# Kernel optimization log

Hardware: AMD Instinct MI355X
Metric: run time of the kernel (lower is better)

The kernel has to match this reference:

```python
import jax, jax.numpy as jnp
import numpy as np

MAX_SENT_LEN = 28
B, LAT, D, E = 2048, 256, 1024, 256
LN_EPS = 1e-5


def setup_inputs() -> dict:
    key = jax.random.key(0)
    ks = jax.random.split(key, 10)
    s = 0.05
    return {
        "z": jax.random.normal(ks[0], (B, LAT), jnp.float32),
        "true_inp": jax.random.normal(ks[1], (B, MAX_SENT_LEN, E), jnp.float32),
        "tf_mask": jax.random.bernoulli(ks[2], 0.5, (MAX_SENT_LEN,)),
        "fc_w": jax.random.normal(ks[3], (D, LAT), jnp.float32) * s,
        "fc_b": jnp.zeros((D,), jnp.float32),
        "ln_w": jnp.ones((D,), jnp.float32),
        "ln_b": jnp.zeros((D,), jnp.float32),
        "w_ih": jax.random.normal(ks[4], (3 * D, D), jnp.float32) * s,
        "b_ih": jnp.zeros((3 * D,), jnp.float32),
        "w_hh": jax.random.normal(ks[5], (3 * D, D), jnp.float32) * s,
        "b_hh": jnp.zeros((3 * D,), jnp.float32),
    }


def reference(z, true_inp, tf_mask, fc_w, fc_b, ln_w, ln_b, w_ih, b_ih, w_hh, b_hh):
    # fc + layer norm -> initial hidden and (repeated) step input, [B, D]
    x = z @ fc_w.T + fc_b
    mu = jnp.mean(x, axis=-1, keepdims=True)
    var = jnp.mean(jnp.square(x - mu), axis=-1, keepdims=True)
    x = (x - mu) * jax.lax.rsqrt(var + LN_EPS) * ln_w + ln_b

    # encoded input is identical at every step -> precompute input gates once
    gi = x @ w_ih.T + b_ih                      # [B, 3D]
    i_r, i_z, i_n = jnp.split(gi, 3, axis=-1)

    # true_inp.repeat(1,1,repeating).transpose(1,0) -> [T, B, D]
    rep = D // E
    true_rep = jnp.transpose(jnp.tile(true_inp, (1, 1, rep)), (1, 0, 2))

    def step(h, inputs):
        t_inp, m = inputs
        h_in = jnp.where(m, t_inp, h)           # teacher-forcing branch
        gh = h_in @ w_hh.T + b_hh               # [B, 3D]
        h_r, h_z, h_n = jnp.split(gh, 3, axis=-1)
        r = jax.nn.sigmoid(i_r + h_r)
        u = jax.nn.sigmoid(i_z + h_z)
        n = jnp.tanh(i_n + r * h_n)
        h_new = (1.0 - u) * n + u * h_in
        return h_new, h_new

    _, outs = jax.lax.scan(step, x, (true_rep, tf_mask))
    return outs                                  # [T, B, D]
```

## Files before the change

### kernel.cpp

```cpp
#include <hip/hip_runtime.h>
#include <hip/hip_bf16.h>

#define TSTEPS 28

typedef __attribute__((ext_vector_type(8))) short bf16x8;
typedef __attribute__((ext_vector_type(4))) float f32x4;
typedef __attribute__((ext_vector_type(4))) unsigned short u16x4;
typedef __hip_bfloat16 bf16;

__device__ __forceinline__ unsigned short f2b(float f) {
  bf16 h = __float2bfloat16(f);
  return *reinterpret_cast<unsigned short*>(&h);
}
__device__ __forceinline__ float b2f(unsigned short u) {
  bf16 h = *reinterpret_cast<bf16*>(&u);
  return __bfloat162float(h);
}

__device__ __forceinline__ void gload16(const void* g, void* l) {
  __builtin_amdgcn_global_load_lds(
      (const __attribute__((address_space(1))) void*)g,
      (__attribute__((address_space(3))) void*)l, 16, 0, 0);
}

__device__ __forceinline__ float sigm(float x) { return 1.f / (1.f + __expf(-x)); }
__device__ __forceinline__ float tanh_fast(float x) {
  const float e2 = __expf(2.f * x);
  return 1.f - 2.f / (e2 + 1.f);
}

__global__ void conv_kernel(const float* __restrict__ in, unsigned short* __restrict__ out, int n4) {
  int i = blockIdx.x * blockDim.x + threadIdx.x;
  const int stride = gridDim.x * blockDim.x;
  for (; i < n4; i += stride) {
    const float4 v = *(const float4*)&in[(size_t)i * 4];
    u16x4 o;
    o.x = f2b(v.x); o.y = f2b(v.y); o.z = f2b(v.z); o.w = f2b(v.w);
    *(u16x4*)&out[(size_t)i * 4] = o;
  }
}

__global__ __launch_bounds__(256) void fold_kernel(const float* __restrict__ whh,
                                                   unsigned short* __restrict__ whf) {
  const int idx = blockIdx.x * 256 + threadIdx.x;
  const int n = idx >> 6, k4 = (idx & 63) << 2;
  const float* r = &whh[(size_t)n * 1024 + k4];
  const float4 a = *(const float4*)r;
  const float4 b = *(const float4*)(r + 256);
  const float4 c = *(const float4*)(r + 512);
  const float4 d = *(const float4*)(r + 768);
  u16x4 o;
  o.x = f2b(a.x + b.x + c.x + d.x);
  o.y = f2b(a.y + b.y + c.y + d.y);
  o.z = f2b(a.z + b.z + c.z + d.z);
  o.w = f2b(a.w + b.w + c.w + d.w);
  *(u16x4*)&whf[(size_t)n * 256 + k4] = o;
}

__global__ __launch_bounds__(256, 2) void gemm_fc_kernel(
    const bf16* __restrict__ A, const bf16* __restrict__ W,
    const float* __restrict__ bias, float* __restrict__ out) {
  constexpr int K = 256, NT = K / 32;
  __shared__ __align__(16) bf16 lds[2][6144];
  const int tid = threadIdx.x;
  const int lane = tid & 63;
  const int l15 = lane & 15, l4 = lane >> 4;
  const int wid = tid >> 6, wm = wid >> 1, wn = wid & 1;
  const int m0 = blockIdx.x * 128, n0 = blockIdx.y * 64;
  const int ra = tid >> 2, cb = (tid & 3) * 8;

  f32x4 acc[4][2] = {};

  auto STAGE = [&](int buf, int kt) {
    const int k0 = kt * 32;
    gload16(&A[(size_t)(m0 + ra) * K + k0 + cb], &lds[buf][tid * 8]);
    gload16(&A[(size_t)(m0 + 64 + ra) * K + k0 + cb], &lds[buf][2048 + tid * 8]);
    gload16(&W[(size_t)(n0 + ra) * K + k0 + cb], &lds[buf][4096 + tid * 8]);
  };

  STAGE(0, 0);
  __syncthreads();
  for (int kt = 0; kt < NT; ++kt) {
    const int buf = kt & 1;
    if (kt + 1 < NT) STAGE(buf ^ 1, kt + 1);
    bf16x8 af[4], bfr[2];
#pragma unroll
    for (int m = 0; m < 4; ++m)
      af[m] = *(const bf16x8*)&lds[buf][(wm * 64 + m * 16 + l15) * 32 + l4 * 8];
#pragma unroll
    for (int n = 0; n < 2; ++n)
      bfr[n] = *(const bf16x8*)&lds[buf][4096 + (wn * 32 + n * 16 + l15) * 32 + l4 * 8];
#pragma unroll
    for (int m = 0; m < 4; ++m)
#pragma unroll
      for (int n = 0; n < 2; ++n)
        acc[m][n] = __builtin_amdgcn_mfma_f32_16x16x32_bf16(af[m], bfr[n], acc[m][n], 0, 0, 0);
    __syncthreads();
  }

#pragma unroll
  for (int m = 0; m < 4; ++m) {
#pragma unroll
    for (int n = 0; n < 2; ++n) {
      const int col = n0 + wn * 32 + n * 16 + l15;
      const int rowb = m0 + wm * 64 + m * 16 + l4 * 4;
      const float bv = bias[col];
#pragma unroll
      for (int r = 0; r < 4; ++r)
        out[(size_t)(rowb + r) * 1024 + col] = acc[m][n][r] + bv;
    }
  }
}

__global__ __launch_bounds__(256) void ln_kernel(const float* __restrict__ x,
                                                 const float* __restrict__ w,
                                                 const float* __restrict__ b,
                                                 bf16* __restrict__ h0b,
                                                 float* __restrict__ h0f) {
  const int row = blockIdx.x, tid = threadIdx.x;
  const float4 v = *(const float4*)&x[(size_t)row * 1024 + tid * 4];
  float vv[4] = {v.x, v.y, v.z, v.w};
  float s = vv[0] + vv[1] + vv[2] + vv[3];
  float sq = vv[0] * vv[0] + vv[1] * vv[1] + vv[2] * vv[2] + vv[3] * vv[3];
#pragma unroll
  for (int off = 32; off; off >>= 1) {
    s += __shfl_down(s, off);
    sq += __shfl_down(sq, off);
  }
  __shared__ float sa[4], sb[4];
  const int lane = tid & 63, wid = tid >> 6;
  if (lane == 0) { sa[wid] = s; sb[wid] = sq; }
  __syncthreads();
  s = sa[0] + sa[1] + sa[2] + sa[3];
  sq = sb[0] + sb[1] + sb[2] + sb[3];
  const float mu = s * (1.f / 1024.f);
  const float var = sq * (1.f / 1024.f) - mu * mu;
  const float rs = rsqrtf(var + 1e-5f);
#pragma unroll
  for (int j = 0; j < 4; ++j) {
    const int c = tid * 4 + j;
    const float xv = (vv[j] - mu) * rs * w[c] + b[c];
    h0b[(size_t)row * 1024 + c] = __float2bfloat16(xv);
    h0f[(size_t)row * 1024 + c] = xv;
  }
}

__global__ __launch_bounds__(256, 2) void gemm_gi_kernel(
    const bf16* __restrict__ A,
    const bf16* __restrict__ W,
    const float* __restrict__ bias,
    unsigned short* __restrict__ out) {
  __shared__ __align__(16) bf16 lds[2][16384];
  const int tid = threadIdx.x;
  const int lane = tid & 63, l15 = lane & 15, l4 = lane >> 4;
  const int wid = tid >> 6;
  const int n0 = blockIdx.x * 64, m0 = blockIdx.y * 64;

  f32x4 acc[3][4] = {};

  auto STAGE = [&](int buf, int kt) {
    const int k0 = kt * 64;
#pragma unroll
    for (int j = 0; j < 2; ++j) {
      const int c = tid + j * 256;
      const int row = c >> 3, kk = ((c & 7) ^ (row & 7)) * 8;
      gload16(&A[(size_t)(m0 + row) * 1024 + k0 + kk], &lds[buf][c * 8]);
    }
#pragma unroll
    for (int j = 0; j < 6; ++j) {
      const int c = tid + j * 256;
      const int row = c >> 3, kk = ((c & 7) ^ (row & 7)) * 8;
      gload16(&W[(size_t)((row >> 6) * 1024 + n0 + (row & 63)) * 1024 + k0 + kk],
              &lds[buf][4096 + c * 8]);
    }
  };

  STAGE(0, 0);
  __syncthreads();
  for (int kt = 0; kt < 16; ++kt) {
    const int buf = kt & 1;
    if (kt + 1 < 16) STAGE(buf ^ 1, kt + 1);
#pragma unroll
    for (int ks = 0; ks < 2; ++ks) {
      const int x = (((ks << 2) | l4) ^ (l15 & 7)) * 8;
      bf16x8 af[4], bfr[3];
#pragma unroll
      for (int m = 0; m < 4; ++m)
        af[m] = *(const bf16x8*)&lds[buf][(m * 16 + l15) * 64 + x];
#pragma unroll
      for (int g = 0; g < 3; ++g)
        bfr[g] = *(const bf16x8*)&lds[buf][4096 + (g * 64 + wid * 16 + l15) * 64 + x];
#pragma unroll
      for (int g = 0; g < 3; ++g)
#pragma unroll
        for (int m = 0; m < 4; ++m)
          acc[g][m] = __builtin_amdgcn_mfma_f32_16x16x32_bf16(af[m], bfr[g], acc[g][m], 0, 0, 0);
    }
    __syncthreads();
  }

  const int col = n0 + wid * 16 + l15;
#pragma unroll
  for (int g = 0; g < 3; ++g) {
    const float bv = bias[g * 1024 + col];
#pragma unroll
    for (int m = 0; m < 4; ++m) {
      const int rowb = m0 + m * 16 + l4 * 4;
#pragma unroll
      for (int r = 0; r < 4; ++r)
        out[(size_t)(rowb + r) * 3072 + g * 1024 + col] = f2b(acc[g][m][r] + bv);
    }
  }
}

__global__ __launch_bounds__(256, 2) void batch_masked_kernel(
    const bf16* __restrict__ trueb,
    const int* __restrict__ tfmask,
    const bf16* __restrict__ whf,
    const float* __restrict__ bhh,
    const unsigned short* __restrict__ gib,
    float* __restrict__ out) {
  const int t = blockIdx.z;
  if (tfmask[t] == 0) return;
  __shared__ __align__(16) bf16 lds[2][16384];
  const int tid = threadIdx.x;
  const int lane = tid & 63, l15 = lane & 15, l4 = lane >> 4;
  const int wid = tid >> 6;
  const int n0 = blockIdx.x * 64, m0 = blockIdx.y * 64;

  f32x4 acc[3][4] = {};

  auto STAGE = [&](int buf, int kt) {
    const int k0 = kt * 64;
#pragma unroll
    for (int j = 0; j < 2; ++j) {
      const int c = tid + j * 256;
      const int row = c >> 3, kk = ((c & 7) ^ (row & 7)) * 8;
      gload16(&trueb[((size_t)(m0 + row) * TSTEPS + t) * 256 + k0 + kk], &lds[buf][c * 8]);
    }
#pragma unroll
    for (int j = 0; j < 6; ++j) {
      const int c = tid + j * 256;
      const int row = c >> 3, kk = ((c & 7) ^ (row & 7)) * 8;
      gload16(&whf[(size_t)((row >> 6) * 1024 + n0 + (row & 63)) * 256 + k0 + kk],
              &lds[buf][4096 + c * 8]);
    }
  };

  STAGE(0, 0);
  __syncthreads();
  for (int kt = 0; kt < 4; ++kt) {
    const int buf = kt & 1;
    if (kt + 1 < 4) STAGE(buf ^ 1, kt + 1);
#pragma unroll
    for (int ks = 0; ks < 2; ++ks) {
      const int x = (((ks << 2) | l4) ^ (l15 & 7)) * 8;
      bf16x8 af[4], bfr[3];
#pragma unroll
      for (int m = 0; m < 4; ++m)
        af[m] = *(const bf16x8*)&lds[buf][(m * 16 + l15) * 64 + x];
#pragma unroll
      for (int g = 0; g < 3; ++g)
        bfr[g] = *(const bf16x8*)&lds[buf][4096 + (g * 64 + wid * 16 + l15) * 64 + x];
#pragma unroll
      for (int g = 0; g < 3; ++g)
#pragma unroll
        for (int m = 0; m < 4; ++m)
          acc[g][m] = __builtin_amdgcn_mfma_f32_16x16x32_bf16(af[m], bfr[g], acc[g][m], 0, 0, 0);
    }
    __syncthreads();
  }

  float* outT = out + (size_t)t * 2048 * 1024;
  const int col = n0 + wid * 16 + l15;
  const float br = bhh[col], bz = bhh[col + 1024], bn_ = bhh[col + 2048];
  const unsigned short* tb = (const unsigned short*)trueb;
#pragma unroll
  for (int m = 0; m < 4; ++m) {
    const int rowb = m0 + m * 16 + l4 * 4;
#pragma unroll
    for (int r = 0; r < 4; ++r) {
      const int row = rowb + r;
      const unsigned short* girow = &gib[(size_t)row * 3072];
      const float ir = b2f(girow[col]), iz = b2f(girow[col + 1024]), inn = b2f(girow[col + 2048]);
      const float hr = acc[0][m][r] + br;
      const float hz = acc[1][m][r] + bz;
      const float hn = acc[2][m][r] + bn_;
      const float hinv = b2f(tb[((size_t)row * TSTEPS + t) * 256 + (col & 255)]);
      const float rg = sigm(ir + hr);
      const float ug = sigm(iz + hz);
      const float ng = tanh_fast(inn + rg * hn);
      outT[(size_t)row * 1024 + col] = (1.f - ug) * ng + ug * hinv;
    }
  }
}

__global__ __launch_bounds__(256, 2) void step_kernel(
    const float* __restrict__ prevf,
    const bf16* __restrict__ hbfprev,
    bf16* __restrict__ hbfout,
    const int* __restrict__ tfmask,
    const bf16* __restrict__ whh,
    const float* __restrict__ bhh,
    const unsigned short* __restrict__ gib,
    float* __restrict__ out, int t) {
  if (tfmask[t] != 0) return;
  const bool predf32 = (t == 0) || (tfmask[t - 1] != 0);
  const int lid = blockIdx.x;
  const int xcd = lid & 7, rest = lid >> 3;
  const int m0 = (rest & 31) * 64;
  const int n0 = ((xcd << 1) | (rest >> 5)) * 64;

  __shared__ __align__(16) bf16 lds[2][16384];
  const int tid = threadIdx.x;
  const int lane = tid & 63, l15 = lane & 15, l4 = lane >> 4;
  const int wid = tid >> 6;

  f32x4 acc[3][4] = {};

  auto STAGE = [&](int buf, int kt) {
    const int k0 = kt * 64;
#pragma unroll
    for (int j = 0; j < 2; ++j) {
      const int c = tid + j * 256;
      const int row = c >> 3, kk = ((c & 7) ^ (row & 7)) * 8;
      if (predf32) {
        const float* src = &prevf[(size_t)(m0 + row) * 1024 + k0 + kk];
        const float4 v0 = *(const float4*)src;
        const float4 v1 = *(const float4*)(src + 4);
        bf16x8 sv;
        sv[0] = (short)f2b(v0.x); sv[1] = (short)f2b(v0.y);
        sv[2] = (short)f2b(v0.z); sv[3] = (short)f2b(v0.w);
        sv[4] = (short)f2b(v1.x); sv[5] = (short)f2b(v1.y);
        sv[6] = (short)f2b(v1.z); sv[7] = (short)f2b(v1.w);
        *(bf16x8*)&lds[buf][c * 8] = sv;
      } else {
        gload16(&hbfprev[(size_t)(m0 + row) * 1024 + k0 + kk], &lds[buf][c * 8]);
      }
    }
#pragma unroll
    for (int j = 0; j < 6; ++j) {
      const int c = tid + j * 256;
      const int row = c >> 3, kk = ((c & 7) ^ (row & 7)) * 8;
      gload16(&whh[(size_t)((row >> 6) * 1024 + n0 + (row & 63)) * 1024 + k0 + kk],
              &lds[buf][4096 + c * 8]);
    }
  };

  STAGE(0, 0);
  __syncthreads();
  for (int kt = 0; kt < 16; ++kt) {
    const int buf = kt & 1;
    if (kt + 1 < 16) STAGE(buf ^ 1, kt + 1);
#pragma unroll
    for (int ks = 0; ks < 2; ++ks) {
      const int x = (((ks << 2) | l4) ^ (l15 & 7)) * 8;
      bf16x8 af[4], bfr[3];
#pragma unroll
      for (int m = 0; m < 4; ++m)
        af[m] = *(const bf16x8*)&lds[buf][(m * 16 + l15) * 64 + x];
#pragma unroll
      for (int g = 0; g < 3; ++g)
        bfr[g] = *(const bf16x8*)&lds[buf][4096 + (g * 64 + wid * 16 + l15) * 64 + x];
#pragma unroll
      for (int g = 0; g < 3; ++g)
#pragma unroll
        for (int m = 0; m < 4; ++m)
          acc[g][m] = __builtin_amdgcn_mfma_f32_16x16x32_bf16(af[m], bfr[g], acc[g][m], 0, 0, 0);
    }
    __syncthreads();
  }

  float* outT = out + (size_t)t * 2048 * 1024;
  const int col = n0 + wid * 16 + l15;
  const float br = bhh[col], bz = bhh[col + 1024], bn_ = bhh[col + 2048];
#pragma unroll
  for (int m = 0; m < 4; ++m) {
    const int rowb = m0 + m * 16 + l4 * 4;
#pragma unroll
    for (int r = 0; r < 4; ++r) {
      const int row = rowb + r;
      const unsigned short* girow = &gib[(size_t)row * 3072];
      const float ir = b2f(girow[col]), iz = b2f(girow[col + 1024]), inn = b2f(girow[col + 2048]);
      const float hr = acc[0][m][r] + br;
      const float hz = acc[1][m][r] + bz;
      const float hn = acc[2][m][r] + bn_;
      const float hinv = prevf[(size_t)row * 1024 + col];
      const float rg = sigm(ir + hr);
      const float ug = sigm(iz + hz);
      const float ng = tanh_fast(inn + rg * hn);
      const float hnew = (1.f - ug) * ng + ug * hinv;
      outT[(size_t)row * 1024 + col] = hnew;
      hbfout[(size_t)row * 1024 + col] = __float2bfloat16(hnew);
    }
  }
}

extern "C" void kernel_launch(void* const* d_in, const int* in_sizes, int n_in,
                              void* d_out, int out_size, void* d_ws, size_t ws_size,
                              hipStream_t stream) {
  (void)in_sizes; (void)n_in; (void)out_size; (void)ws_size;
  const float* z = (const float*)d_in[0];
  const float* trueinp = (const float*)d_in[1];
  const int* tfmask = (const int*)d_in[2];
  const float* fc_w = (const float*)d_in[3];
  const float* fc_b = (const float*)d_in[4];
  const float* ln_w = (const float*)d_in[5];
  const float* ln_b = (const float*)d_in[6];
  const float* w_ih = (const float*)d_in[7];
  const float* b_ih = (const float*)d_in[8];
  const float* w_hh = (const float*)d_in[9];
  const float* b_hh = (const float*)d_in[10];
  float* out = (float*)d_out;

  char* ws = (char*)d_ws;
  size_t o = 0;
  float* xraw = (float*)(ws + o); o += (size_t)2048 * 1024 * 4;
  float* h0f  = (float*)(ws + o); o += (size_t)2048 * 1024 * 4;
  unsigned short* gib = (unsigned short*)(ws + o); o += (size_t)2048 * 3072 * 2;
  bf16* h0b   = (bf16*)(ws + o);  o += (size_t)2048 * 1024 * 2;
  bf16* hbf0  = (bf16*)(ws + o);  o += (size_t)2048 * 1024 * 2;
  bf16* hbf1  = (bf16*)(ws + o);  o += (size_t)2048 * 1024 * 2;
  bf16* zb    = (bf16*)(ws + o);  o += (size_t)2048 * 256 * 2;
  bf16* fcwb  = (bf16*)(ws + o);  o += (size_t)1024 * 256 * 2;
  bf16* wihb  = (bf16*)(ws + o);  o += (size_t)3072 * 1024 * 2;
  bf16* whhb  = (bf16*)(ws + o);  o += (size_t)3072 * 1024 * 2;
  bf16* whf   = (bf16*)(ws + o);  o += (size_t)3072 * 256 * 2;
  bf16* trueb = (bf16*)(ws + o);  o += (size_t)2048 * TSTEPS * 256 * 2;

  conv_kernel<<<1024, 256, 0, stream>>>(z, (unsigned short*)zb, 2048 * 256 / 4);
  conv_kernel<<<512, 256, 0, stream>>>(fc_w, (unsigned short*)fcwb, 1024 * 256 / 4);
  conv_kernel<<<2048, 256, 0, stream>>>(w_ih, (unsigned short*)wihb, 3072 * 1024 / 4);
  conv_kernel<<<2048, 256, 0, stream>>>(w_hh, (unsigned short*)whhb, 3072 * 1024 / 4);
  conv_kernel<<<2048, 256, 0, stream>>>(trueinp, (unsigned short*)trueb, 2048 * TSTEPS * 256 / 4);
  fold_kernel<<<768, 256, 0, stream>>>(w_hh, (unsigned short*)whf);

  gemm_fc_kernel<<<dim3(16, 16), 256, 0, stream>>>(zb, fcwb, fc_b, xraw);
  ln_kernel<<<2048, 256, 0, stream>>>(xraw, ln_w, ln_b, h0b, h0f);
  gemm_gi_kernel<<<dim3(16, 32), 256, 0, stream>>>(h0b, wihb, b_ih, gib);

  batch_masked_kernel<<<dim3(16, 32, TSTEPS), 256, 0, stream>>>(trueb, tfmask, whf,
                                                                b_hh, gib, out);

  const float* prev = h0f;
  for (int t = 0; t < TSTEPS; ++t) {
    bf16* hw = (t & 1) ? hbf1 : hbf0;
    const bf16* hr = (t & 1) ? hbf0 : hbf1;
    step_kernel<<<512, 256, 0, stream>>>(prev, hr, hw, tfmask, whhb, b_hh, gib, out, t);
    prev = out + (size_t)t * 2048 * 1024;
  }
}
```

Baseline: 589.0 us.

## Replace per-step kernel launches with one persistent cooperative kernel using grid sync

Measured after the change: 1.445 ms. 2.45x slower.

```diff
diff --git a/kernel.cpp b/kernel.cpp
--- a/kernel.cpp
+++ b/kernel.cpp
@@ -1,5 +1,8 @@
 #include <hip/hip_runtime.h>
 #include <hip/hip_bf16.h>
+#include <hip/hip_cooperative_groups.h>
+
+namespace cg = cooperative_groups;
 
 #define TSTEPS 28
 
@@ -392,6 +395,125 @@
       const float hnew = (1.f - ug) * ng + ug * hinv;
       outT[(size_t)row * 1024 + col] = hnew;
       hbfout[(size_t)row * 1024 + col] = __float2bfloat16(hnew);
+    }
+  }
+}
+
+__global__ __launch_bounds__(256, 1) void chain_kernel(
+    const float* __restrict__ h0f,
+    bf16* __restrict__ hbf0, bf16* __restrict__ hbf1,
+    const int* __restrict__ tfmask,
+    const bf16* __restrict__ whh,
+    const float* __restrict__ bhh,
+    const unsigned short* __restrict__ gib,
+    float* __restrict__ out) {
+  cg::grid_group grid = cg::this_grid();
+  const int lid = blockIdx.x;
+  const int xcd = lid & 7, rest = lid >> 3;
+  const int n0 = ((xcd << 1) | (rest >> 4)) * 64;
+  const int mbase = rest & 15;
+
+  __shared__ __align__(16) bf16 lds[2][16384];
+  const int tid = threadIdx.x;
+  const int lane = tid & 63, l15 = lane & 15, l4 = lane >> 4;
+  const int wid = tid >> 6;
+
+  for (int t = 0; t < TSTEPS; ++t) {
+    if (tfmask[t] != 0) continue;
+    if (t > 0 && tfmask[t - 1] == 0) {
+      __threadfence();
+      grid.sync();
+      __threadfence();
+    }
+    const bool predf32 = (t == 0) || (tfmask[t - 1] != 0);
+    const float* prevf = (t == 0) ? h0f : out + (size_t)(t - 1) * 2048 * 1024;
+    const bf16* hbfprev = (t & 1) ? hbf0 : hbf1;
+    bf16* hbfout = (t & 1) ? hbf1 : hbf0;
+    float* outT = out + (size_t)t * 2048 * 1024;
+
+    auto STAGE = [&](int buf, int m0, int kt) {
+      const int k0 = kt * 64;
+#pragma unroll
+      for (int j = 0; j < 2; ++j) {
+        const int c = tid + j * 256;
+        const int row = c >> 3, kk = ((c & 7) ^ (row & 7)) * 8;
+        if (predf32) {
+          const float* src = &prevf[(size_t)(m0 + row) * 1024 + k0 + kk];
+          const float4 v0 = *(const float4*)src;
+          const float4 v1 = *(const float4*)(src + 4);
+          bf16x8 sv;
+          sv[0] = (short)f2b(v0.x); sv[1] = (short)f2b(v0.y);
+          sv[2] = (short)f2b(v0.z); sv[3] = (short)f2b(v0.w);
+          sv[4] = (short)f2b(v1.x); sv[5] = (short)f2b(v1.y);
+          sv[6] = (short)f2b(v1.z); sv[7] = (short)f2b(v1.w);
+          *(bf16x8*)&lds[buf][c * 8] = sv;
+        } else {
+          gload16(&hbfprev[(size_t)(m0 + row) * 1024 + k0 + kk], &lds[buf][c * 8]);
+        }
+      }
+#pragma unroll
+      for (int j = 0; j < 6; ++j) {
+        const int c = tid + j * 256;
+        const int row = c >> 3, kk = ((c & 7) ^ (row & 7)) * 8;
+        gload16(&whh[(size_t)((row >> 6) * 1024 + n0 + (row & 63)) * 1024 + k0 + kk],
+                &lds[buf][4096 + c * 8]);
+      }
+    };
+
+    int m0 = mbase * 64;
+    STAGE(0, m0, 0);
+#pragma unroll
+    for (int tl = 0; tl < 2; ++tl) {
+      __syncthreads();
+      f32x4 acc[3][4] = {};
+      for (int kt = 0; kt < 16; ++kt) {
+        const int buf = kt & 1;
+        if (kt + 1 < 16) STAGE(buf ^ 1, m0, kt + 1);
+#pragma unroll
+        for (int ks = 0; ks < 2; ++ks) {
+          const int x = (((ks << 2) | l4) ^ (l15 & 7)) * 8;
+          bf16x8 af[4], bfr[3];
+#pragma unroll
+          for (int m = 0; m < 4; ++m)
+            af[m] = *(const bf16x8*)&lds[buf][(m * 16 + l15) * 64 + x];
+#pragma unroll
+          for (int g = 0; g < 3; ++g)
+            bfr[g] = *(const bf16x8*)&lds[buf][4096 + (g * 64 + wid * 16 + l15) * 64 + x];
+#pragma unroll
+          for (int g = 0; g < 3; ++g)
+#pragma unroll
+            for (int m = 0; m < 4; ++m)
+              acc[g][m] = __builtin_amdgcn_mfma_f32_16x16x32_bf16(af[m], bfr[g], acc[g][m], 0, 0, 0);
+        }
+        __syncthreads();
+      }
+      const int m0_done = m0;
+      if (tl == 0) {
+        m0 = (mbase + 16) * 64;
+        STAGE(0, m0, 0);
+      }
+      const int col = n0 + wid * 16 + l15;
+      const float br = bhh[col], bz = bhh[col + 1024], bn_ = bhh[col + 2048];
+#pragma unroll
+      for (int m = 0; m < 4; ++m) {
+        const int rowb = m0_done + m * 16 + l4 * 4;
+#pragma unroll
+        for (int r = 0; r < 4; ++r) {
+          const int row = rowb + r;
+          const unsigned short* girow = &gib[(size_t)row * 3072];
+          const float ir = b2f(girow[col]), iz = b2f(girow[col + 1024]), inn = b2f(girow[col + 2048]);
+          const float hr = acc[0][m][r] + br;
+          const float hz = acc[1][m][r] + bz;
+          const float hn = acc[2][m][r] + bn_;
+          const float hinv = prevf[(size_t)row * 1024 + col];
+          const float rg = sigm(ir + hr);
+          const float ug = sigm(iz + hz);
+          const float ng = tanh_fast(inn + rg * hn);
+          const float hnew = (1.f - ug) * ng + ug * hinv;
+          outT[(size_t)row * 1024 + col] = hnew;
+          hbfout[(size_t)row * 1024 + col] = __float2bfloat16(hnew);
+        }
+      }
     }
   }
 }
@@ -442,11 +564,28 @@
   batch_masked_kernel<<<dim3(16, 32, TSTEPS), 256, 0, stream>>>(trueb, tfmask, whf,
                                                                 b_hh, gib, out);
 
-  const float* prev = h0f;
-  for (int t = 0; t < TSTEPS; ++t) {
-    bf16* hw = (t & 1) ? hbf1 : hbf0;
-    const bf16* hr = (t & 1) ? hbf0 : hbf1;
-    step_kernel<<<512, 256, 0, stream>>>(prev, hr, hw, tfmask, whhb, b_hh, gib, out, t);
-    prev = out + (size_t)t * 2048 * 1024;
-  }
-}
+  {
+    const float* a0 = h0f;
+    bf16* a1 = hbf0;
+    bf16* a2 = hbf1;
+    const int* a3 = tfmask;
+    const bf16* a4 = whhb;
+    const float* a5 = b_hh;
+    const unsigned short* a6 = gib;
+    float* a7 = out;
+    void* args[] = {(void*)&a0, (void*)&a1, (void*)&a2, (void*)&a3,
+                    (void*)&a4, (void*)&a5, (void*)&a6, (void*)&a7};
+    hipError_t err = hipLaunchCooperativeKernel((void*)chain_kernel, dim3(256), dim3(256),
+                                                args, 0, stream);
+    if (err != hipSuccess) {
+      (void)hipGetLastError();
+      const float* prev = h0f;
+      for (int t = 0; t < TSTEPS; ++t) {
+        bf16* hw = (t & 1) ? hbf1 : hbf0;
+        const bf16* hr = (t & 1) ? hbf0 : hbf1;
+        step_kernel<<<512, 256, 0, stream>>>(prev, hr, hw, tfmask, whhb, b_hh, gib, out, t);
+        prev = out + (size_t)t * 2048 * 1024;
+      }
+    }
+  }
+}
```

## Use 8-wave blocks for GRU GEMMs and fuse fp32→bf16 conversion into staging

Applied to the files above, without the earlier changes.

New measurement: 525.1 us. 10.9% less time.

```diff
diff --git a/kernel.cpp b/kernel.cpp
--- a/kernel.cpp
+++ b/kernel.cpp
@@ -27,6 +27,17 @@
 __device__ __forceinline__ float tanh_fast(float x) {
   const float e2 = __expf(2.f * x);
   return 1.f - 2.f / (e2 + 1.f);
+}
+
+__device__ __forceinline__ bf16x8 cvt8(const float* src) {
+  const float4 v0 = *(const float4*)src;
+  const float4 v1 = *(const float4*)(src + 4);
+  bf16x8 sv;
+  sv[0] = (short)f2b(v0.x); sv[1] = (short)f2b(v0.y);
+  sv[2] = (short)f2b(v0.z); sv[3] = (short)f2b(v0.w);
+  sv[4] = (short)f2b(v1.x); sv[5] = (short)f2b(v1.y);
+  sv[6] = (short)f2b(v1.z); sv[7] = (short)f2b(v1.w);
+  return sv;
 }
 
 __global__ void conv_kernel(const float* __restrict__ in, unsigned short* __restrict__ out, int n4) {
@@ -58,7 +69,7 @@
 }
 
 __global__ __launch_bounds__(256, 2) void gemm_fc_kernel(
-    const bf16* __restrict__ A, const bf16* __restrict__ W,
+    const float* __restrict__ A, const float* __restrict__ W,
     const float* __restrict__ bias, float* __restrict__ out) {
   constexpr int K = 256, NT = K / 32;
   __shared__ __align__(16) bf16 lds[2][6144];
@@ -73,9 +84,9 @@
 
   auto STAGE = [&](int buf, int kt) {
     const int k0 = kt * 32;
-    gload16(&A[(size_t)(m0 + ra) * K + k0 + cb], &lds[buf][tid * 8]);
-    gload16(&A[(size_t)(m0 + 64 + ra) * K + k0 + cb], &lds[buf][2048 + tid * 8]);
-    gload16(&W[(size_t)(n0 + ra) * K + k0 + cb], &lds[buf][4096 + tid * 8]);
+    *(bf16x8*)&lds[buf][tid * 8]        = cvt8(&A[(size_t)(m0 + ra) * K + k0 + cb]);
+    *(bf16x8*)&lds[buf][2048 + tid * 8] = cvt8(&A[(size_t)(m0 + 64 + ra) * K + k0 + cb]);
+    *(bf16x8*)&lds[buf][4096 + tid * 8] = cvt8(&W[(size_t)(n0 + ra) * K + k0 + cb]);
   };
 
   STAGE(0, 0);
@@ -145,33 +156,32 @@
   }
 }
 
-__global__ __launch_bounds__(256, 2) void gemm_gi_kernel(
+__global__ __launch_bounds__(512, 4) void gemm_gi_kernel(
     const bf16* __restrict__ A,
-    const bf16* __restrict__ W,
+    const float* __restrict__ W,
     const float* __restrict__ bias,
     unsigned short* __restrict__ out) {
   __shared__ __align__(16) bf16 lds[2][16384];
   const int tid = threadIdx.x;
   const int lane = tid & 63, l15 = lane & 15, l4 = lane >> 4;
-  const int wid = tid >> 6;
+  const int wid = tid >> 6, wm = wid >> 2, wn = wid & 3;
   const int n0 = blockIdx.x * 64, m0 = blockIdx.y * 64;
 
-  f32x4 acc[3][4] = {};
+  f32x4 acc[3][2] = {};
 
   auto STAGE = [&](int buf, int kt) {
     const int k0 = kt * 64;
-#pragma unroll
-    for (int j = 0; j < 2; ++j) {
-      const int c = tid + j * 256;
+    {
+      const int c = tid;
       const int row = c >> 3, kk = ((c & 7) ^ (row & 7)) * 8;
       gload16(&A[(size_t)(m0 + row) * 1024 + k0 + kk], &lds[buf][c * 8]);
     }
 #pragma unroll
-    for (int j = 0; j < 6; ++j) {
-      const int c = tid + j * 256;
-      const int row = c >> 3, kk = ((c & 7) ^ (row & 7)) * 8;
-      gload16(&W[(size_t)((row >> 6) * 1024 + n0 + (row & 63)) * 1024 + k0 + kk],
-              &lds[buf][4096 + c * 8]);
+    for (int j = 0; j < 3; ++j) {
+      const int c = tid + j * 512;
+      const int row = c >> 3, kk = ((c & 7) ^ (row & 7)) * 8;
+      *(bf16x8*)&lds[buf][4096 + c * 8] =
+          cvt8(&W[(size_t)((row >> 6) * 1024 + n0 + (row & 63)) * 1024 + k0 + kk]);
     }
   };
 
@@ -183,29 +193,29 @@
 #pragma unroll
     for (int ks = 0; ks < 2; ++ks) {
       const int x = (((ks << 2) | l4) ^ (l15 & 7)) * 8;
-      bf16x8 af[4], bfr[3];
-#pragma unroll
-      for (int m = 0; m < 4; ++m)
-        af[m] = *(const bf16x8*)&lds[buf][(m * 16 + l15) * 64 + x];
-#pragma unroll
-      for (int g = 0; g < 3; ++g)
-        bfr[g] = *(const bf16x8*)&lds[buf][4096 + (g * 64 + wid * 16 + l15) * 64 + x];
-#pragma unroll
-      for (int g = 0; g < 3; ++g)
-#pragma unroll
-        for (int m = 0; m < 4; ++m)
+      bf16x8 af[2], bfr[3];
+#pragma unroll
+      for (int m = 0; m < 2; ++m)
+        af[m] = *(const bf16x8*)&lds[buf][(wm * 32 + m * 16 + l15) * 64 + x];
+#pragma unroll
+      for (int g = 0; g < 3; ++g)
+        bfr[g] = *(const bf16x8*)&lds[buf][4096 + (g * 64 + wn * 16 + l15) * 64 + x];
+#pragma unroll
+      for (int g = 0; g < 3; ++g)
+#pragma unroll
+        for (int m = 0; m < 2; ++m)
           acc[g][m] = __builtin_amdgcn_mfma_f32_16x16x32_bf16(af[m], bfr[g], acc[g][m], 0, 0, 0);
     }
     __syncthreads();
   }
 
-  const int col = n0 + wid * 16 + l15;
+  const int col = n0 + wn * 16 + l15;
 #pragma unroll
   for (int g = 0; g < 3; ++g) {
     const float bv = bias[g * 1024 + col];
 #pragma unroll
-    for (int m = 0; m < 4; ++m) {
-      const int rowb = m0 + m * 16 + l4 * 4;
+    for (int m = 0; m < 2; ++m) {
+      const int rowb = m0 + wm * 32 + m * 16 + l4 * 4;
 #pragma unroll
       for (int r = 0; r < 4; ++r)
         out[(size_t)(rowb + r) * 3072 + g * 1024 + col] = f2b(acc[g][m][r] + bv);
@@ -213,7 +223,7 @@
   }
 }
 
-__global__ __launch_bounds__(256, 2) void batch_masked_kernel(
+__global__ __launch_bounds__(512, 4) void batch_masked_kernel(
     const bf16* __restrict__ trueb,
     const int* __restrict__ tfmask,
     const bf16* __restrict__ whf,
@@ -225,22 +235,21 @@
   __shared__ __align__(16) bf16 lds[2][16384];
   const int tid = threadIdx.x;
   const int lane = tid & 63, l15 = lane & 15, l4 = lane >> 4;
-  const int wid = tid >> 6;
+  const int wid = tid >> 6, wm = wid >> 2, wn = wid & 3;
   const int n0 = blockIdx.x * 64, m0 = blockIdx.y * 64;
 
-  f32x4 acc[3][4] = {};
+  f32x4 acc[3][2] = {};
 
   auto STAGE = [&](int buf, int kt) {
     const int k0 = kt * 64;
-#pragma unroll
-    for (int j = 0; j < 2; ++j) {
-      const int c = tid + j * 256;
+    {
+      const int c = tid;
       const int row = c >> 3, kk = ((c & 7) ^ (row & 7)) * 8;
       gload16(&trueb[((size_t)(m0 + row) * TSTEPS + t) * 256 + k0 + kk], &lds[buf][c * 8]);
     }
 #pragma unroll
-    for (int j = 0; j < 6; ++j) {
-      const int c = tid + j * 256;
+    for (int j = 0; j < 3; ++j) {
+      const int c = tid + j * 512;
       const int row = c >> 3, kk = ((c & 7) ^ (row & 7)) * 8;
       gload16(&whf[(size_t)((row >> 6) * 1024 + n0 + (row & 63)) * 256 + k0 + kk],
               &lds[buf][4096 + c * 8]);
@@ -255,29 +264,29 @@
 #pragma unroll
     for (int ks = 0; ks < 2; ++ks) {
       const int x = (((ks << 2) | l4) ^ (l15 & 7)) * 8;
-      bf16x8 af[4], bfr[3];
-#pragma unroll
-      for (int m = 0; m < 4; ++m)
-        af[m] = *(const bf16x8*)&lds[buf][(m * 16 + l15) * 64 + x];
-#pragma unroll
-      for (int g = 0; g < 3; ++g)
-        bfr[g] = *(const bf16x8*)&lds[buf][4096 + (g * 64 + wid * 16 + l15) * 64 + x];
-#pragma unroll
-      for (int g = 0; g < 3; ++g)
-#pragma unroll
-        for (int m = 0; m < 4; ++m)
+      bf16x8 af[2], bfr[3];
+#pragma unroll
+      for (int m = 0; m < 2; ++m)
+        af[m] = *(const bf16x8*)&lds[buf][(wm * 32 + m * 16 + l15) * 64 + x];
+#pragma unroll
+      for (int g = 0; g < 3; ++g)
+        bfr[g] = *(const bf16x8*)&lds[buf][4096 + (g * 64 + wn * 16 + l15) * 64 + x];
+#pragma unroll
+      for (int g = 0; g < 3; ++g)
+#pragma unroll
+        for (int m = 0; m < 2; ++m)
           acc[g][m] = __builtin_amdgcn_mfma_f32_16x16x32_bf16(af[m], bfr[g], acc[g][m], 0, 0, 0);
     }
     __syncthreads();
   }
 
   float* outT = out + (size_t)t * 2048 * 1024;
-  const int col = n0 + wid * 16 + l15;
+  const int col = n0 + wn * 16 + l15;
   const float br = bhh[col], bz = bhh[col + 1024], bn_ = bhh[col + 2048];
   const unsigned short* tb = (const unsigned short*)trueb;
 #pragma unroll
-  for (int m = 0; m < 4; ++m) {
-    const int rowb = m0 + m * 16 + l4 * 4;
+  for (int m = 0; m < 2; ++m) {
+    const int rowb = m0 + wm * 32 + m * 16 + l4 * 4;
 #pragma unroll
     for (int r = 0; r < 4; ++r) {
       const int row = rowb + r;
@@ -295,7 +304,7 @@
   }
 }
 
-__global__ __launch_bounds__(256, 2) void step_kernel(
+__global__ __launch_bounds__(512, 4) void step_kernel(
     const float* __restrict__ prevf,
     const bf16* __restrict__ hbfprev,
     bf16* __restrict__ hbfout,
@@ -314,33 +323,24 @@
   __shared__ __align__(16) bf16 lds[2][16384];
   const int tid = threadIdx.x;
   const int lane = tid & 63, l15 = lane & 15, l4 = lane >> 4;
-  const int wid = tid >> 6;
-
-  f32x4 acc[3][4] = {};
+  const int wid = tid >> 6, wm = wid >> 2, wn = wid & 3;
+
+  f32x4 acc[3][2] = {};
 
   auto STAGE = [&](int buf, int kt) {
     const int k0 = kt * 64;
-#pragma unroll
-    for (int j = 0; j < 2; ++j) {
-      const int c = tid + j * 256;
+    {
+      const int c = tid;
       const int row = c >> 3, kk = ((c & 7) ^ (row & 7)) * 8;
       if (predf32) {
-        const float* src = &prevf[(size_t)(m0 + row) * 1024 + k0 + kk];
-        const float4 v0 = *(const float4*)src;
-        const float4 v1 = *(const float4*)(src + 4);
-        bf16x8 sv;
-        sv[0] = (short)f2b(v0.x); sv[1] = (short)f2b(v0.y);
-        sv[2] = (short)f2b(v0.z); sv[3] = (short)f2b(v0.w);
-        sv[4] = (short)f2b(v1.x); sv[5] = (short)f2b(v1.y);
-        sv[6] = (short)f2b(v1.z); sv[7] = (short)f2b(v1.w);
-        *(bf16x8*)&lds[buf][c * 8] = sv;
+        *(bf16x8*)&lds[buf][c * 8] = cvt8(&prevf[(size_t)(m0 + row) * 1024 + k0 + kk]);
       } else {
         gload16(&hbfprev[(size_t)(m0 + row) * 1024 + k0 + kk], &lds[buf][c * 8]);
       }
     }
 #pragma unroll
-    for (int j = 0; j < 6; ++j) {
-      const int c = tid + j * 256;
+    for (int j = 0; j < 3; ++j) {
+      const int c = tid + j * 512;
       const int row = c >> 3, kk = ((c & 7) ^ (row & 7)) * 8;
       gload16(&whh[(size_t)((row >> 6) * 1024 + n0 + (row & 63)) * 1024 + k0 + kk],
               &lds[buf][4096 + c * 8]);
@@ -355,28 +355,28 @@
 #pragma unroll
     for (int ks = 0; ks < 2; ++ks) {
       const int x = (((ks << 2) | l4) ^ (l15 & 7)) * 8;
-      bf16x8 af[4], bfr[3];
-#pragma unroll
-      for (int m = 0; m < 4; ++m)
-        af[m] = *(const bf16x8*)&lds[buf][(m * 16 + l15) * 64 + x];
-#pragma unroll
-      for (int g = 0; g < 3; ++g)
-        bfr[g] = *(const bf16x8*)&lds[buf][4096 + (g * 64 + wid * 16 + l15) * 64 + x];
-#pragma unroll
-      for (int g = 0; g < 3; ++g)
-#pragma unroll
-        for (int m = 0; m < 4; ++m)
+      bf16x8 af[2], bfr[3];
+#pragma unroll
+      for (int m = 0; m < 2; ++m)
+        af[m] = *(const bf16x8*)&lds[buf][(wm * 32 + m * 16 + l15) * 64 + x];
+#pragma unroll
+      for (int g = 0; g < 3; ++g)
+        bfr[g] = *(const bf16x8*)&lds[buf][4096 + (g * 64 + wn * 16 + l15) * 64 + x];
+#pragma unroll
+      for (int g = 0; g < 3; ++g)
+#pragma unroll
+        for (int m = 0; m < 2; ++m)
           acc[g][m] = __builtin_amdgcn_mfma_f32_16x16x32_bf16(af[m], bfr[g], acc[g][m], 0, 0, 0);
     }
     __syncthreads();
   }
 
   float* outT = out + (size_t)t * 2048 * 1024;
-  const int col = n0 + wid * 16 + l15;
+  const int col = n0 + wn * 16 + l15;
   const float br = bhh[col], bz = bhh[col + 1024], bn_ = bhh[col + 2048];
 #pragma unroll
-  for (int m = 0; m < 4; ++m) {
-    const int rowb = m0 + m * 16 + l4 * 4;
+  for (int m = 0; m < 2; ++m) {
+    const int rowb = m0 + wm * 32 + m * 16 + l4 * 4;
 #pragma unroll
     for (int r = 0; r < 4; ++r) {
       const int row = rowb + r;
@@ -421,32 +421,26 @@
   bf16* h0b   = (bf16*)(ws + o);  o += (size_t)2048 * 1024 * 2;
   bf16* hbf0  = (bf16*)(ws + o);  o += (size_t)2048 * 1024 * 2;
   bf16* hbf1  = (bf16*)(ws + o);  o += (size_t)2048 * 1024 * 2;
-  bf16* zb    = (bf16*)(ws + o);  o += (size_t)2048 * 256 * 2;
-  bf16* fcwb  = (bf16*)(ws + o);  o += (size_t)1024 * 256 * 2;
-  bf16* wihb  = (bf16*)(ws + o);  o += (size_t)3072 * 1024 * 2;
   bf16* whhb  = (bf16*)(ws + o);  o += (size_t)3072 * 1024 * 2;
   bf16* whf   = (bf16*)(ws + o);  o += (size_t)3072 * 256 * 2;
   bf16* trueb = (bf16*)(ws + o);  o += (size_t)2048 * TSTEPS * 256 * 2;
 
-  conv_kernel<<<1024, 256, 0, stream>>>(z, (unsigned short*)zb, 2048 * 256 / 4);
-  conv_kernel<<<512, 256, 0, stream>>>(fc_w, (unsigned short*)fcwb, 1024 * 256 / 4);
-  conv_kernel<<<2048, 256, 0, stream>>>(w_ih, (unsigned short*)wihb, 3072 * 1024 / 4);
   conv_kernel<<<2048, 256, 0, stream>>>(w_hh, (unsigned short*)whhb, 3072 * 1024 / 4);
   conv_kernel<<<2048, 256, 0, stream>>>(trueinp, (unsigned short*)trueb, 2048 * TSTEPS * 256 / 4);
   fold_kernel<<<768, 256, 0, stream>>>(w_hh, (unsigned short*)whf);
 
-  gemm_fc_kernel<<<dim3(16, 16), 256, 0, stream>>>(zb, fcwb, fc_b, xraw);
+  gemm_fc_kernel<<<dim3(16, 16), 256, 0, stream>>>(z, fc_w, fc_b, xraw);
   ln_kernel<<<2048, 256, 0, stream>>>(xraw, ln_w, ln_b, h0b, h0f);
-  gemm_gi_kernel<<<dim3(16, 32), 256, 0, stream>>>(h0b, wihb, b_ih, gib);
-
-  batch_masked_kernel<<<dim3(16, 32, TSTEPS), 256, 0, stream>>>(trueb, tfmask, whf,
+  gemm_gi_kernel<<<dim3(16, 32), 512, 0, stream>>>(h0b, w_ih, b_ih, gib);
+
+  batch_masked_kernel<<<dim3(16, 32, TSTEPS), 512, 0, stream>>>(trueb, tfmask, whf,
                                                                 b_hh, gib, out);
 
   const float* prev = h0f;
   for (int t = 0; t < TSTEPS; ++t) {
     bf16* hw = (t & 1) ? hbf1 : hbf0;
     const bf16* hr = (t & 1) ? hbf0 : hbf1;
-    step_kernel<<<512, 256, 0, stream>>>(prev, hr, hw, tfmask, whhb, b_hh, gib, out, t);
+    step_kernel<<<512, 512, 0, stream>>>(prev, hr, hw, tfmask, whhb, b_hh, gib, out, t);
     prev = out + (size_t)t * 2048 * 1024;
   }
 }
```
